# Kernel tuning notes

Measured on AMD Instinct MI355X. Metric: run time of the kernel, lower is better.

The kernel has to match this reference:

```python
import jax, jax.numpy as jnp
import numpy as np

QMIN_A, QMAX_A = -128, 127  # int8 activation range
GROUPSIZE = 32


def per_token_quant_dequant(x):
    """Dynamic per-token asymmetric int8 fake-quant (torchao per_token_dynamic_quant)."""
    min_val = jnp.minimum(jnp.min(x, axis=-1, keepdims=True), 0.0)
    max_val = jnp.maximum(jnp.max(x, axis=-1, keepdims=True), 0.0)
    scale = (max_val - min_val) / float(QMAX_A - QMIN_A)
    scale = jnp.maximum(scale, jnp.finfo(x.dtype).eps)
    zp = jnp.clip(QMIN_A - jnp.round(min_val / scale), QMIN_A, QMAX_A)
    q = jnp.clip(jnp.round(x / scale) + zp, QMIN_A, QMAX_A)
    return (q - zp) * scale


def dequant_int4_grouped(w_int, w_scales, w_zeros):
    """w_int: [O, I] int4 values in [-8, 7]; scales/zeros: [O, I//GROUPSIZE]."""
    O, I = w_int.shape
    G = I // GROUPSIZE
    wg = w_int.reshape(O, G, GROUPSIZE).astype(w_scales.dtype)
    w_dq = (wg - w_zeros[:, :, None]) * w_scales[:, :, None]
    return w_dq.reshape(O, I)


def setup_inputs() -> dict:
    key = jax.random.key(0)
    k1, k2, k3 = jax.random.split(key, 3)
    B, S, D_IN, D_OUT = 4, 2048, 2048, 2048
    G = D_IN // GROUPSIZE
    x = jax.random.normal(k1, (B, S, D_IN), dtype=jnp.float32)
    w_int = jax.random.randint(k2, (D_OUT, D_IN), -8, 8, dtype=jnp.int32)
    w_scales = jax.random.uniform(k3, (D_OUT, G), dtype=jnp.float32) * 0.01 + 1e-3
    w_zeros = jnp.zeros((D_OUT, G), dtype=jnp.float32)
    return {"x": x, "w_int": w_int, "w_scales": w_scales, "w_zeros": w_zeros}


def reference(x, w_int, w_scales, w_zeros):
    x_dq = per_token_quant_dequant(x)                  # [B, S, I]
    w_dq = dequant_int4_grouped(w_int, w_scales, w_zeros)  # [O, I]
    return jnp.einsum("bsi,oi->bso", x_dq, w_dq)       # [B, S, O]
```

## Files before the change

kernel.cpp:

```cpp
#include <hip/hip_runtime.h>

#define M_DIM 8192
#define N_DIM 2048
#define K_DIM 2048

#define BM 128
#define BN 128
#define BK 32

#define AS1 __attribute__((address_space(1)))
#define AS3 __attribute__((address_space(3)))

typedef float f32x4 __attribute__((ext_vector_type(4)));
typedef short s16x8 __attribute__((ext_vector_type(8)));

__device__ __forceinline__ unsigned short f2bf(float f) {
  unsigned int u = __float_as_uint(f);
  u += 0x7FFFu + ((u >> 16) & 1u);
  return (unsigned short)(u >> 16);
}

__global__ __launch_bounds__(256) void quant_x_kernel(
    const float* __restrict__ x, unsigned short* __restrict__ A) {
  const int t   = blockIdx.x;
  const int tid = threadIdx.x;
  const float4* r4 = (const float4*)(x + (size_t)t * K_DIM);
  float4 v0 = r4[tid];
  float4 v1 = r4[tid + 256];

  float mn = fminf(fminf(fminf(v0.x, v0.y), fminf(v0.z, v0.w)),
                   fminf(fminf(v1.x, v1.y), fminf(v1.z, v1.w)));
  float mx = fmaxf(fmaxf(fmaxf(v0.x, v0.y), fmaxf(v0.z, v0.w)),
                   fmaxf(fmaxf(v1.x, v1.y), fmaxf(v1.z, v1.w)));
#pragma unroll
  for (int off = 32; off > 0; off >>= 1) {
    mn = fminf(mn, __shfl_xor(mn, off));
    mx = fmaxf(mx, __shfl_xor(mx, off));
  }
  __shared__ float smn[4], smx[4];
  if ((tid & 63) == 0) { smn[tid >> 6] = mn; smx[tid >> 6] = mx; }
  __syncthreads();
  mn = fminf(fminf(smn[0], smn[1]), fminf(smn[2], smn[3]));
  mx = fmaxf(fmaxf(smx[0], smx[1]), fmaxf(smx[2], smx[3]));
  mn = fminf(mn, 0.0f);
  mx = fmaxf(mx, 0.0f);

  float scale = (mx - mn) / 255.0f;
  scale = fmaxf(scale, 1.1920928955078125e-07f);
  float zp = -128.0f - rintf(mn / scale);
  zp = fminf(fmaxf(zp, -128.0f), 127.0f);

  ushort4* Ao = (ushort4*)(A + (size_t)t * K_DIM);
  {
    float q; ushort4 r;
    q = rintf(v0.x / scale) + zp; q = fminf(fmaxf(q, -128.f), 127.f); r.x = f2bf((q - zp) * scale);
    q = rintf(v0.y / scale) + zp; q = fminf(fmaxf(q, -128.f), 127.f); r.y = f2bf((q - zp) * scale);
    q = rintf(v0.z / scale) + zp; q = fminf(fmaxf(q, -128.f), 127.f); r.z = f2bf((q - zp) * scale);
    q = rintf(v0.w / scale) + zp; q = fminf(fmaxf(q, -128.f), 127.f); r.w = f2bf((q - zp) * scale);
    Ao[tid] = r;
  }
  {
    float q; ushort4 r;
    q = rintf(v1.x / scale) + zp; q = fminf(fmaxf(q, -128.f), 127.f); r.x = f2bf((q - zp) * scale);
    q = rintf(v1.y / scale) + zp; q = fminf(fmaxf(q, -128.f), 127.f); r.y = f2bf((q - zp) * scale);
    q = rintf(v1.z / scale) + zp; q = fminf(fmaxf(q, -128.f), 127.f); r.z = f2bf((q - zp) * scale);
    q = rintf(v1.w / scale) + zp; q = fminf(fmaxf(q, -128.f), 127.f); r.w = f2bf((q - zp) * scale);
    Ao[tid + 256] = r;
  }
}

__global__ __launch_bounds__(256) void prep_w_kernel(
    const int* __restrict__ w, const float* __restrict__ ws,
    const float* __restrict__ wz, unsigned short* __restrict__ W) {
  const int idx = blockIdx.x * 256 + threadIdx.x;
  const int o  = idx >> 8;
  const int ii = (idx & 255) * 8;
  const int g  = ii >> 5;
  const float s = ws[o * 64 + g];
  const float z = wz[o * 64 + g];
  const int4* wp = (const int4*)(w + (size_t)o * K_DIM + ii);
  int4 a = wp[0], b = wp[1];
  ushort4 r0, r1;
  r0.x = f2bf(((float)a.x - z) * s);
  r0.y = f2bf(((float)a.y - z) * s);
  r0.z = f2bf(((float)a.z - z) * s);
  r0.w = f2bf(((float)a.w - z) * s);
  r1.x = f2bf(((float)b.x - z) * s);
  r1.y = f2bf(((float)b.y - z) * s);
  r1.z = f2bf(((float)b.z - z) * s);
  r1.w = f2bf(((float)b.w - z) * s);
  ushort4* Wo = (ushort4*)(W + (size_t)o * K_DIM + ii);
  Wo[0] = r0;
  Wo[1] = r1;
}

__global__ __launch_bounds__(256) void gemm_kernel(
    const unsigned short* __restrict__ A,
    const unsigned short* __restrict__ B,
    float* __restrict__ C) {
  __shared__ unsigned short As[BM * BK];
  __shared__ unsigned short Bs[BN * BK];

  const int tid  = threadIdx.x;
  const int bm   = blockIdx.y * BM;
  const int bn   = blockIdx.x * BN;
  const int lane = tid & 63;
  const int wv   = tid >> 6;
  const int waveM = (wv >> 1) * 64;
  const int waveN = (wv & 1) * 64;
  const int quad = lane >> 4;
  const int l16  = lane & 15;

  const int srow0 = tid >> 2;
  const int srow1 = 64 + (tid >> 2);
  const int kcp   = tid & 3;
  const int kc0   = kcp ^ ((srow0 >> 1) & 3);
  const int kc1   = kcp ^ ((srow1 >> 1) & 3);

  const unsigned short* ag0 = A + (size_t)(bm + srow0) * K_DIM + kc0 * 8;
  const unsigned short* ag1 = A + (size_t)(bm + srow1) * K_DIM + kc1 * 8;
  const unsigned short* bg0 = B + (size_t)(bn + srow0) * K_DIM + kc0 * 8;
  const unsigned short* bg1 = B + (size_t)(bn + srow1) * K_DIM + kc1 * 8;

  unsigned short* la0 = &As[tid * 8];
  unsigned short* la1 = &As[2048 + tid * 8];
  unsigned short* lb0 = &Bs[tid * 8];
  unsigned short* lb1 = &Bs[2048 + tid * 8];

  int aoff[4], boff[4];
#pragma unroll
  for (int i = 0; i < 4; ++i) {
    int ra = waveM + i * 16 + l16;
    aoff[i] = ra * BK + (quad ^ ((ra >> 1) & 3)) * 8;
    int rb = waveN + i * 16 + l16;
    boff[i] = rb * BK + (quad ^ ((rb >> 1) & 3)) * 8;
  }

  f32x4 acc[4][4] = {};

  for (int k0 = 0; k0 < K_DIM; k0 += BK) {
    __builtin_amdgcn_global_load_lds((const AS1 void*)(ag0 + k0), (AS3 void*)la0, 16, 0, 0);
    __builtin_amdgcn_global_load_lds((const AS1 void*)(ag1 + k0), (AS3 void*)la1, 16, 0, 0);
    __builtin_amdgcn_global_load_lds((const AS1 void*)(bg0 + k0), (AS3 void*)lb0, 16, 0, 0);
    __builtin_amdgcn_global_load_lds((const AS1 void*)(bg1 + k0), (AS3 void*)lb1, 16, 0, 0);
    __syncthreads();

    s16x8 af[4], bf[4];
#pragma unroll
    for (int i = 0; i < 4; ++i) {
      af[i] = *(const s16x8*)&As[aoff[i]];
      bf[i] = *(const s16x8*)&Bs[boff[i]];
    }
#pragma unroll
    for (int mi = 0; mi < 4; ++mi)
#pragma unroll
      for (int ni = 0; ni < 4; ++ni)
        acc[mi][ni] = __builtin_amdgcn_mfma_f32_16x16x32_bf16(
            af[mi], bf[ni], acc[mi][ni], 0, 0, 0);
    __syncthreads();
  }

#pragma unroll
  for (int mi = 0; mi < 4; ++mi) {
#pragma unroll
    for (int ni = 0; ni < 4; ++ni) {
      const int o = bn + waveN + ni * 16 + l16;
#pragma unroll
      for (int r = 0; r < 4; ++r) {
        const int t = bm + waveM + mi * 16 + quad * 4 + r;
        C[(size_t)t * N_DIM + o] = acc[mi][ni][r];
      }
    }
  }
}

extern "C" void kernel_launch(void* const* d_in, const int* in_sizes, int n_in,
                              void* d_out, int out_size, void* d_ws, size_t ws_size,
                              hipStream_t stream) {
  const float* x        = (const float*)d_in[0];
  const int*   w_int    = (const int*)d_in[1];
  const float* w_scales = (const float*)d_in[2];
  const float* w_zeros  = (const float*)d_in[3];
  float* out = (float*)d_out;

  unsigned short* Aq = (unsigned short*)d_ws;
  unsigned short* Wq = Aq + (size_t)M_DIM * K_DIM;

  quant_x_kernel<<<M_DIM, 256, 0, stream>>>(x, Aq);
  prep_w_kernel<<<(N_DIM * (K_DIM / 8)) / 256, 256, 0, stream>>>(w_int, w_scales, w_zeros, Wq);
  dim3 grid(N_DIM / BN, M_DIM / BM);
  gemm_kernel<<<grid, 256, 0, stream>>>(Aq, Wq, out);
}
```

Baseline: 227.6 us.

## Enlarge GEMM tile to 256x128x64 with 8-way XOR swizzle and reciprocal quant

The GEMM block tile grows from 128x128 to 256x128 and the K step from 32 to 64. Each wave now computes a 128x64 sub-tile with 32 accumulators, and the LDS swizzle is reworked to an 8-chunk XOR pattern. The aim is more MFMA work per global load and per barrier, with half as many K-loop iterations. In exchange it uses more registers and LDS, and asks for 2 blocks per CU via launch bounds, which could force spills or lower occupancy. The quant kernel also replaces per-element division by scale with multiplication by a precomputed reciprocal, which can shift rounding slightly.

```diff
diff --git a/kernel.cpp b/kernel.cpp
--- a/kernel.cpp
+++ b/kernel.cpp
@@ -4,9 +4,9 @@
 #define N_DIM 2048
 #define K_DIM 2048
 
-#define BM 128
+#define BM 256
 #define BN 128
-#define BK 32
+#define BK 64
 
 #define AS1 __attribute__((address_space(1)))
 #define AS3 __attribute__((address_space(3)))
@@ -47,24 +47,25 @@
 
   float scale = (mx - mn) / 255.0f;
   scale = fmaxf(scale, 1.1920928955078125e-07f);
-  float zp = -128.0f - rintf(mn / scale);
+  const float inv = 1.0f / scale;
+  float zp = -128.0f - rintf(mn * inv);
   zp = fminf(fmaxf(zp, -128.0f), 127.0f);
 
   ushort4* Ao = (ushort4*)(A + (size_t)t * K_DIM);
   {
     float q; ushort4 r;
-    q = rintf(v0.x / scale) + zp; q = fminf(fmaxf(q, -128.f), 127.f); r.x = f2bf((q - zp) * scale);
-    q = rintf(v0.y / scale) + zp; q = fminf(fmaxf(q, -128.f), 127.f); r.y = f2bf((q - zp) * scale);
-    q = rintf(v0.z / scale) + zp; q = fminf(fmaxf(q, -128.f), 127.f); r.z = f2bf((q - zp) * scale);
-    q = rintf(v0.w / scale) + zp; q = fminf(fmaxf(q, -128.f), 127.f); r.w = f2bf((q - zp) * scale);
+    q = rintf(v0.x * inv) + zp; q = fminf(fmaxf(q, -128.f), 127.f); r.x = f2bf((q - zp) * scale);
+    q = rintf(v0.y * inv) + zp; q = fminf(fmaxf(q, -128.f), 127.f); r.y = f2bf((q - zp) * scale);
+    q = rintf(v0.z * inv) + zp; q = fminf(fmaxf(q, -128.f), 127.f); r.z = f2bf((q - zp) * scale);
+    q = rintf(v0.w * inv) + zp; q = fminf(fmaxf(q, -128.f), 127.f); r.w = f2bf((q - zp) * scale);
     Ao[tid] = r;
   }
   {
     float q; ushort4 r;
-    q = rintf(v1.x / scale) + zp; q = fminf(fmaxf(q, -128.f), 127.f); r.x = f2bf((q - zp) * scale);
-    q = rintf(v1.y / scale) + zp; q = fminf(fmaxf(q, -128.f), 127.f); r.y = f2bf((q - zp) * scale);
-    q = rintf(v1.z / scale) + zp; q = fminf(fmaxf(q, -128.f), 127.f); r.z = f2bf((q - zp) * scale);
-    q = rintf(v1.w / scale) + zp; q = fminf(fmaxf(q, -128.f), 127.f); r.w = f2bf((q - zp) * scale);
+    q = rintf(v1.x * inv) + zp; q = fminf(fmaxf(q, -128.f), 127.f); r.x = f2bf((q - zp) * scale);
+    q = rintf(v1.y * inv) + zp; q = fminf(fmaxf(q, -128.f), 127.f); r.y = f2bf((q - zp) * scale);
+    q = rintf(v1.z * inv) + zp; q = fminf(fmaxf(q, -128.f), 127.f); r.z = f2bf((q - zp) * scale);
+    q = rintf(v1.w * inv) + zp; q = fminf(fmaxf(q, -128.f), 127.f); r.w = f2bf((q - zp) * scale);
     Ao[tid + 256] = r;
   }
 }
@@ -94,7 +95,7 @@
   Wo[1] = r1;
 }
 
-__global__ __launch_bounds__(256) void gemm_kernel(
+__global__ __launch_bounds__(256, 2) void gemm_kernel(
     const unsigned short* __restrict__ A,
     const unsigned short* __restrict__ B,
     float* __restrict__ C) {
@@ -106,62 +107,60 @@
   const int bn   = blockIdx.x * BN;
   const int lane = tid & 63;
   const int wv   = tid >> 6;
-  const int waveM = (wv >> 1) * 64;
+  const int waveM = (wv >> 1) * 128;
   const int waveN = (wv & 1) * 64;
   const int quad = lane >> 4;
   const int l16  = lane & 15;
 
-  const int srow0 = tid >> 2;
-  const int srow1 = 64 + (tid >> 2);
-  const int kcp   = tid & 3;
-  const int kc0   = kcp ^ ((srow0 >> 1) & 3);
-  const int kc1   = kcp ^ ((srow1 >> 1) & 3);
+  const int trow = tid >> 3;
+  const int phys = (tid & 7) ^ (trow & 7);
+  const unsigned short* ag = A + (size_t)(bm + trow) * K_DIM + phys * 8;
+  const unsigned short* bg = B + (size_t)(bn + trow) * K_DIM + phys * 8;
+  unsigned short* al = &As[tid * 8];
+  unsigned short* bl = &Bs[tid * 8];
 
-  const unsigned short* ag0 = A + (size_t)(bm + srow0) * K_DIM + kc0 * 8;
-  const unsigned short* ag1 = A + (size_t)(bm + srow1) * K_DIM + kc1 * 8;
-  const unsigned short* bg0 = B + (size_t)(bn + srow0) * K_DIM + kc0 * 8;
-  const unsigned short* bg1 = B + (size_t)(bn + srow1) * K_DIM + kc1 * 8;
+  int aoff[8], boff[4];
+#pragma unroll
+  for (int mi = 0; mi < 8; ++mi)
+    aoff[mi] = (waveM + mi * 16 + l16) * BK + ((quad ^ (l16 & 7)) * 8);
+#pragma unroll
+  for (int ni = 0; ni < 4; ++ni)
+    boff[ni] = (waveN + ni * 16 + l16) * BK + ((quad ^ (l16 & 7)) * 8);
 
-  unsigned short* la0 = &As[tid * 8];
-  unsigned short* la1 = &As[2048 + tid * 8];
-  unsigned short* lb0 = &Bs[tid * 8];
-  unsigned short* lb1 = &Bs[2048 + tid * 8];
-
-  int aoff[4], boff[4];
-#pragma unroll
-  for (int i = 0; i < 4; ++i) {
-    int ra = waveM + i * 16 + l16;
-    aoff[i] = ra * BK + (quad ^ ((ra >> 1) & 3)) * 8;
-    int rb = waveN + i * 16 + l16;
-    boff[i] = rb * BK + (quad ^ ((rb >> 1) & 3)) * 8;
-  }
-
-  f32x4 acc[4][4] = {};
+  f32x4 acc[8][4] = {};
 
   for (int k0 = 0; k0 < K_DIM; k0 += BK) {
-    __builtin_amdgcn_global_load_lds((const AS1 void*)(ag0 + k0), (AS3 void*)la0, 16, 0, 0);
-    __builtin_amdgcn_global_load_lds((const AS1 void*)(ag1 + k0), (AS3 void*)la1, 16, 0, 0);
-    __builtin_amdgcn_global_load_lds((const AS1 void*)(bg0 + k0), (AS3 void*)lb0, 16, 0, 0);
-    __builtin_amdgcn_global_load_lds((const AS1 void*)(bg1 + k0), (AS3 void*)lb1, 16, 0, 0);
+#pragma unroll
+    for (int j = 0; j < 8; ++j)
+      __builtin_amdgcn_global_load_lds((const AS1 void*)(ag + (size_t)j * 32 * K_DIM + k0),
+                                       (AS3 void*)(al + j * 2048), 16, 0, 0);
+#pragma unroll
+    for (int j = 0; j < 4; ++j)
+      __builtin_amdgcn_global_load_lds((const AS1 void*)(bg + (size_t)j * 32 * K_DIM + k0),
+                                       (AS3 void*)(bl + j * 2048), 16, 0, 0);
     __syncthreads();
 
-    s16x8 af[4], bf[4];
 #pragma unroll
-    for (int i = 0; i < 4; ++i) {
-      af[i] = *(const s16x8*)&As[aoff[i]];
-      bf[i] = *(const s16x8*)&Bs[boff[i]];
-    }
+    for (int kk = 0; kk < 2; ++kk) {
+      s16x8 af[8], bf[4];
 #pragma unroll
-    for (int mi = 0; mi < 4; ++mi)
+      for (int mi = 0; mi < 8; ++mi)
+        af[mi] = *(const s16x8*)&As[aoff[mi] ^ (kk * 32)];
 #pragma unroll
       for (int ni = 0; ni < 4; ++ni)
-        acc[mi][ni] = __builtin_amdgcn_mfma_f32_16x16x32_bf16(
-            af[mi], bf[ni], acc[mi][ni], 0, 0, 0);
+        bf[ni] = *(const s16x8*)&Bs[boff[ni] ^ (kk * 32)];
+#pragma unroll
+      for (int mi = 0; mi < 8; ++mi)
+#pragma unroll
+        for (int ni = 0; ni < 4; ++ni)
+          acc[mi][ni] = __builtin_amdgcn_mfma_f32_16x16x32_bf16(
+              af[mi], bf[ni], acc[mi][ni], 0, 0, 0);
+    }
     __syncthreads();
   }
 
 #pragma unroll
-  for (int mi = 0; mi < 4; ++mi) {
+  for (int mi = 0; mi < 8; ++mi) {
 #pragma unroll
     for (int ni = 0; ni < 4; ++ni) {
       const int o = bn + waveN + ni * 16 + l16;
```

Result: faster. 195.1 us (-14.3%).
